# Optimization experiments

Measured on AMD Instinct MI355X. Metric: run time of the kernel, lower is better.

The kernel has to match this reference:

```python
import jax, jax.numpy as jnp
import numpy as np

B, C, N, T = 32, 32, 300, 64      # batch, residual/conv channels, nodes, seq_len
DIM, K, SKIP, GD = 40, 20, 64, 2  # node_dim, top-k (subgraph_size), skip_channels, gcn_depth
TANH_A, PROP_A = 3.0, 0.05
KSET = (2, 3, 6, 7)
TOUT = T - (KSET[-1] - 1)          # 58: time length after dilated inception (dilation=1)


def conv2d(x, w, b):
    y = jax.lax.conv_general_dilated(x, w, (1, 1), 'VALID', dimension_numbers=('NCHW', 'OIHW', 'NCHW'))
    return y + b[None, :, None, None]


def setup_inputs() -> dict:
    key = jax.random.key(0)
    ks = iter(jax.random.split(key, 48))
    def nrm(shape, s=1.0):
        return jax.random.normal(next(ks), shape, jnp.float32) * s
    inp = {
        'x': nrm((B, C, N, T)),
        'x_skip': nrm((B, SKIP, N, 1)),
        'idx': jnp.arange(N, dtype=jnp.int32),
        'emb1': nrm((N, DIM), 0.1), 'emb2': nrm((N, DIM), 0.1),
        'lin1_w': nrm((DIM, DIM), 0.15), 'lin1_b': jnp.zeros((DIM,), jnp.float32),
        'lin2_w': nrm((DIM, DIM), 0.15), 'lin2_b': jnp.zeros((DIM,), jnp.float32),
        'skip_w': nrm((SKIP, C, 1, TOUT), 0.05), 'skip_b': jnp.zeros((SKIP,), jnp.float32),
        'mp1_w': nrm((C, (GD + 1) * C, 1, 1), 0.1), 'mp1_b': jnp.zeros((C,), jnp.float32),
        'mp2_w': nrm((C, (GD + 1) * C, 1, 1), 0.1), 'mp2_b': jnp.zeros((C,), jnp.float32),
        'ln_w': jnp.ones((C, N, TOUT), jnp.float32), 'ln_b': jnp.zeros((C, N, TOUT), jnp.float32),
    }
    for k in KSET:
        inp[f'fw{k}'] = nrm((C // 4, C, 1, k), 0.1); inp[f'fb{k}'] = jnp.zeros((C // 4,), jnp.float32)
        inp[f'gw{k}'] = nrm((C // 4, C, 1, k), 0.1); inp[f'gb{k}'] = jnp.zeros((C // 4,), jnp.float32)
    return inp


def _forward(x, x_skip, idx, emb1, emb2, lin1_w, lin1_b, lin2_w, lin2_b,
             fws, gws, skip_w, skip_b, mp1_w, mp1_b, mp2_w, mp2_b, ln_w, ln_b):
    # --- GraphConstructor: learned sparse adjacency via tanh/relu/top-k/scatter ---
    n1 = jnp.tanh(TANH_A * (emb1[idx] @ lin1_w.T + lin1_b))
    n2 = jnp.tanh(TANH_A * (emb2[idx] @ lin2_w.T + lin2_b))
    a = n1 @ n2.T - n2 @ n1.T
    A = jax.nn.relu(jnp.tanh(TANH_A * a))
    _, cols = jax.lax.top_k(A, K)                               # [N, K] per-row top-k indices
    mask = jnp.zeros_like(A).at[jnp.arange(N)[:, None], cols].set(1.0)
    A = A * mask
    # --- DilatedInception filter/gate (Conv2d kernel (1,k), crop to shortest) ---
    Xf = jnp.tanh(jnp.concatenate([conv2d(x, w, b)[..., -TOUT:] for w, b in fws], axis=1))
    Xg = jax.nn.sigmoid(jnp.concatenate([conv2d(x, w, b)[..., -TOUT:] for w, b in gws], axis=1))
    X = Xf * Xg                                                 # dropout is identity (training=False)
    X_skip_out = conv2d(X, skip_w, skip_b) + x_skip             # [B, SKIP, N, 1]
    # --- MixProp graph diffusion over A and A^T ---
    def mixprop(Xin, Adj, w, b):
        Ah = Adj + jnp.eye(N, dtype=Adj.dtype)
        Ah = Ah / Ah.sum(1)[:, None]                            # row-normalize
        H, hops = Xin, [Xin]
        for _ in range(GD):
            H = PROP_A * Xin + (1.0 - PROP_A) * jnp.einsum('bcwt,vw->bcvt', H, Ah)
            hops.append(H)
        return conv2d(jnp.concatenate(hops, axis=1), w, b)      # 1x1 conv: (GD+1)*C -> C
    X = mixprop(X, A, mp1_w, mp1_b) + mixprop(X, A.T, mp2_w, mp2_b)
    X = X + x[..., -TOUT:]
    # --- LayerNorm over (C, N, TOUT) with node-indexed affine ---
    mu = X.mean(axis=(1, 2, 3), keepdims=True)
    var = ((X - mu) ** 2).mean(axis=(1, 2, 3), keepdims=True)
    Xn = (X - mu) * jax.lax.rsqrt(var + 1e-5)
    X = Xn * ln_w[:, idx, :][None] + ln_b[:, idx, :][None]
    return X, X_skip_out


def reference(x, x_skip, idx, emb1, emb2, lin1_w, lin1_b, lin2_w, lin2_b,
              fw2, fb2, fw3, fb3, fw6, fb6, fw7, fb7,
              gw2, gb2, gw3, gb3, gw6, gb6, gw7, gb7,
              skip_w, skip_b, mp1_w, mp1_b, mp2_w, mp2_b, ln_w, ln_b):
    fws = [(fw2, fb2), (fw3, fb3), (fw6, fb6), (fw7, fb7)]
    gws = [(gw2, gb2), (gw3, gb3), (gw6, gb6), (gw7, gb7)]
    return _forward(x, x_skip, idx, emb1, emb2, lin1_w, lin1_b, lin2_w, lin2_b,
                    fws, gws, skip_w, skip_b, mp1_w, mp1_b, mp2_w, mp2_b, ln_w, ln_b)
```

## Files before the change

kernel.cpp:

```cpp
#include <hip/hip_runtime.h>
#include <hip/hip_bf16.h>
#include <math.h>

typedef __hip_bfloat16 bf16;
typedef __attribute__((ext_vector_type(8))) short bf16x8;
typedef __attribute__((ext_vector_type(4))) float f32x4;

#define NB 32
#define NC 32
#define NNODE 300
#define NT 64
#define NDIM 40
#define KTOP 20
#define NSKIP 64
#define NTOUT 58
#define SLAB 17400
#define BSLAB 556800
#define XEL 17817600
#define PSLAB 2048
#define BPSLAB 614400
#define XPEL 19660800

__device__ __forceinline__ float b2f(bf16 v){ return __bfloat162float(v); }
__device__ __forceinline__ bf16 f2b(float v){ return __float2bfloat16(v); }
__device__ __forceinline__ float fsig(float x){ return 1.0f/(1.0f + __expf(-x)); }
__device__ __forceinline__ float ftanh(float x){ return 2.0f*fsig(2.0f*x) - 1.0f; }

__device__ __forceinline__ unsigned short bbits(float v){
  bf16 h = f2b(v); unsigned short s; __builtin_memcpy(&s, &h, 2); return s;
}

__device__ __forceinline__ uint4 pack8(const float f[8]){
  uint4 d;
  d.x = (unsigned)bbits(f[0]) | ((unsigned)bbits(f[1]) << 16);
  d.y = (unsigned)bbits(f[2]) | ((unsigned)bbits(f[3]) << 16);
  d.z = (unsigned)bbits(f[4]) | ((unsigned)bbits(f[5]) << 16);
  d.w = (unsigned)bbits(f[6]) | ((unsigned)bbits(f[7]) << 16);
  return d;
}

__device__ __forceinline__ void bv_swz(int bid, int& b, int& v){
  int xcd = bid & 7, i = bid >> 3;
  int nb = xcd*1200 + i;
  b = nb / NNODE; v = nb - b*NNODE;
}

__global__ void k_nodes(const float* __restrict__ emb1, const float* __restrict__ emb2,
                        const float* __restrict__ l1w, const float* __restrict__ l1b,
                        const float* __restrict__ l2w, const float* __restrict__ l2b,
                        const int* __restrict__ idxp,
                        float* __restrict__ n1, float* __restrict__ n2){
  int i = blockIdx.x; int d = threadIdx.x;
  if (d >= NDIM) return;
  int r = idxp[i];
  float a1 = l1b[d], a2 = l2b[d];
  for (int k=0;k<NDIM;++k){
    a1 = fmaf(emb1[r*NDIM+k], l1w[d*NDIM+k], a1);
    a2 = fmaf(emb2[r*NDIM+k], l2w[d*NDIM+k], a2);
  }
  n1[i*NDIM+d] = tanhf(3.0f*a1);
  n2[i*NDIM+d] = tanhf(3.0f*a2);
}

__global__ void __launch_bounds__(64) k_adjrow(const float* __restrict__ n1,
                                               const float* __restrict__ n2,
                                               float* __restrict__ Am){
  int i = blockIdx.x; int lane = threadIdx.x;
  __shared__ float rowo[NNODE];
  __shared__ float rowv[NNODE];
  __shared__ int   sel[NNODE];
  for (int j=lane;j<NNODE;j+=64){
    float a = 0.f;
    #pragma unroll
    for (int k=0;k<NDIM;++k){
      float a1 = n1[i*NDIM+k], a2 = n2[i*NDIM+k];
      a = fmaf(a1, n2[j*NDIM+k], a);
      a = fmaf(-a2, n1[j*NDIM+k], a);
    }
    float v = tanhf(3.0f*a);
    v = v > 0.f ? v : 0.f;
    rowo[j]=v; rowv[j]=v; sel[j]=0;
  }
  __syncthreads();
  for (int it=0; it<KTOP; ++it){
    float best = -1.f; int bi = 0x7fffffff;
    for (int j=lane;j<NNODE;j+=64){
      float v = rowv[j];
      if (v > best){ best=v; bi=j; }
    }
    #pragma unroll
    for (int off=32; off; off>>=1){
      float ov = __shfl_xor(best, off);
      int   oi = __shfl_xor(bi, off);
      if (ov > best || (ov == best && oi < bi)){ best=ov; bi=oi; }
    }
    if (lane==0){ sel[bi]=1; rowv[bi]=-2.f; }
    __syncthreads();
  }
  for (int j=lane;j<NNODE;j+=64)
    Am[i*NNODE+j] = sel[j] ? rowo[j] : 0.f;
}

__global__ void __launch_bounds__(64) k_norm(const float* __restrict__ Am, float* __restrict__ Ah){
  int r = blockIdx.x;
  int side = r >= 304; int v = side ? r - 304 : r;
  float* dst = Ah + (size_t)(side ? 304*304 : 0) + v*304;
  int lane = threadIdx.x;
  if (v >= NNODE){
    for (int w=lane; w<304; w+=64) dst[w] = 0.f;
    return;
  }
  float s = 0.f;
  for (int w=lane; w<NNODE; w+=64)
    s += side ? Am[w*NNODE + v] : Am[v*NNODE + w];
  #pragma unroll
  for (int off=32; off; off>>=1) s += __shfl_xor(s, off);
  float inv = 1.0f/(s + 1.0f);
  for (int w=lane; w<304; w+=64){
    float a = (w < NNODE) ? (side ? Am[w*NNODE + v] : Am[v*NNODE + w]) : 0.f;
    if (w == v) a += 1.0f;
    dst[w] = a*inv;
  }
}

__global__ void k_mpk(const float* __restrict__ Ah, bf16* __restrict__ Mpk){
  int id = blockIdx.x*blockDim.x + threadIdx.x;
  if (id >= 4*320*320) return;
  int pm = id / (320*320);
  int rem = id % (320*320);
  int v = rem / 320, w = rem % 320;
  int s = pm >> 1, m = pm & 1;
  float val = 0.f;
  if (v < 304 && w < 304){
    const float* A = Ah + (size_t)s*304*304;
    float a = A[v*304 + w];
    if (m == 0){
      val = 0.95f*a + (v==w ? 0.05f : 0.f);
    } else {
      float d = 0.f;
      for (int u=0; u<304; ++u) d = fmaf(A[v*304 + u], A[u*304 + w], d);
      val = 0.9025f*d + 0.0475f*a + (v==w ? 0.05f : 0.f);
    }
  }
  int vt16 = v >> 4, lv = v & 15, ks = w >> 5, g = (w >> 3) & 3, j = w & 7;
  int lane = g*16 + lv;
  Mpk[(((size_t)(pm*20 + vt16)*10 + ks)*64 + lane)*8 + j] = f2b(val);
}

__global__ void k_wpack2(const float* __restrict__ fw2,const float* __restrict__ fw3,
                         const float* __restrict__ fw6,const float* __restrict__ fw7,
                         const float* __restrict__ gw2,const float* __restrict__ gw3,
                         const float* __restrict__ gw6,const float* __restrict__ gw7,
                         const float* __restrict__ fb2,const float* __restrict__ fb3,
                         const float* __restrict__ fb6,const float* __restrict__ fb7,
                         const float* __restrict__ gb2,const float* __restrict__ gb3,
                         const float* __restrict__ gb6,const float* __restrict__ gb7,
                         bf16* __restrict__ wfA, float* __restrict__ biasPk){
  int T = blockIdx.x*blockDim.x + threadIdx.x;
  if (T < 14336){
    int j = T & 7;
    int q = T >> 3;
    int l = q & 63; q >>= 6;
    int ks = q % 7, mt = q / 7;
    int m = mt*16 + (l & 15);
    int k = ks*32 + (l >> 4)*8 + j;
    int c = m >> 1, path = m & 1;
    int cls = c >> 3, o = c & 7;
    int ic = k / 7, d = k - ic*7;
    int kk = (cls==0) ? 2 : (cls==1) ? 3 : (cls==2) ? 6 : 7;
    int tp = d - (7 - kk);
    float val = 0.f;
    if (tp >= 0){
      const float* w = (path==0)
        ? (cls==0?fw2:cls==1?fw3:cls==2?fw6:fw7)
        : (cls==0?gw2:cls==1?gw3:cls==2?gw6:gw7);
      val = w[(o*NC + ic)*kk + tp];
    }
    wfA[T] = f2b(val);
  } else if (T < 14336 + 32){
    int c = T - 14336;
    int cls = c >> 3, o = c & 7;
    const float* fb = cls==0?fb2:cls==1?fb3:cls==2?fb6:fb7;
    const float* gb = cls==0?gb2:cls==1?gb3:cls==2?gb6:gb7;
    biasPk[c*2]   = fb[o];
    biasPk[c*2+1] = gb[o];
  }
}

__global__ void k_wprepM(const float* __restrict__ m1w, const float* __restrict__ m2w,
                         const float* __restrict__ m1b, const float* __restrict__ m2b,
                         bf16* __restrict__ pkB0, bf16* __restrict__ pkB1,
                         float* __restrict__ biasSum){
  int id = blockIdx.x*blockDim.x + threadIdx.x;
  if (id < 3072){
    int j = id & 7, l = (id >> 3) & 63, q = id >> 9;
    int ks = q % 3, nt = q / 3;
    int k = (l >> 4)*8 + j;
    int c = nt*16 + (l & 15);
    float val;
    if      (ks == 0) val = m1w[c*96 + k] + m2w[c*96 + k];
    else if (ks == 1) val = m1w[c*96 + 32 + k];
    else              val = m1w[c*96 + 64 + k];
    pkB0[id] = f2b(val);
  } else if (id < 5120){
    int id2 = id - 3072;
    int j = id2 & 7, l = (id2 >> 3) & 63, q = id2 >> 9;
    int ks = q & 1, nt = q >> 1;
    int k = (l >> 4)*8 + j;
    int c = nt*16 + (l & 15);
    pkB1[id2] = f2b(ks==0 ? m2w[c*96 + 32 + k] : m2w[c*96 + 64 + k]);
  } else if (id < 5152){
    int c = id - 5120;
    biasSum[c] = m1b[c] + m2b[c];
  }
}

__global__ void k_wTb(const float* __restrict__ sw, bf16* __restrict__ wTb){
  int id = blockIdx.x*blockDim.x + threadIdx.x;
  if (id >= 131072) return;
  int j = id & 7, l = (id >> 3) & 63, q = id >> 9;
  int ks = q & 63, nt = q >> 6;
  int k = ks*32 + (l >> 4)*8 + j;
  int t = k >> 5, c = k & 31;
  int sc = nt*16 + (l & 15);
  float val = (t < NTOUT) ? sw[sc*1856 + c*NTOUT + t] : 0.f;
  wTb[id] = f2b(val);
}

__global__ void __launch_bounds__(256) k_incepM(const float* __restrict__ x,
    const bf16* __restrict__ wfA, const float* __restrict__ biasPk,
    bf16* __restrict__ Xp){
  __shared__ bf16 xsb[32*72];
  __shared__ uint4 xim2[28*64];
  int b, n; bv_swz(blockIdx.x, b, n);
  int bn = b*NNODE + n;
  int tid = threadIdx.x;
  {
    int c = tid >> 3, t0 = (tid & 7)*8;
    const float* src = x + ((size_t)(b*NC + c)*NNODE + n)*NT + t0;
    float4 v0 = *reinterpret_cast<const float4*>(src);
    float4 v1 = *reinterpret_cast<const float4*>(src + 4);
    float f[8] = {v0.x,v0.y,v0.z,v0.w,v1.x,v1.y,v1.z,v1.w};
    *reinterpret_cast<uint4*>(&xsb[c*72 + t0]) = pack8(f);
    if ((tid & 7) == 7)
      *reinterpret_cast<uint4*>(&xsb[c*72 + 64]) = make_uint4(0,0,0,0);
  }
  __syncthreads();
  #pragma unroll
  for (int i=0;i<7;++i){
    int pr = tid + i*256;
    int kb = pr >> 6, t = pr & 63;
    int k0 = kb*8;
    int ic = k0 / 7, d = k0 - ic*7;
    unsigned sh[8];
    #pragma unroll
    for (int j=0;j<8;++j){
      sh[j] = *reinterpret_cast<const unsigned short*>(&xsb[ic*72 + t + d]);
      ++d; if (d == 7){ d = 0; ++ic; }
    }
    xim2[kb*64 + t] = make_uint4(sh[0]|(sh[1]<<16), sh[2]|(sh[3]<<16),
                                 sh[4]|(sh[5]<<16), sh[6]|(sh[7]<<16));
  }
  __syncthreads();
  int lane = tid & 63;
  int mt = __builtin_amdgcn_readfirstlane(tid >> 6);
  bf16x8 wA[7];
  #pragma unroll
  for (int ks=0; ks<7; ++ks)
    wA[ks] = *reinterpret_cast<const bf16x8*>(wfA + (size_t)((mt*7 + ks)*64 + lane)*8);
  int g = lane >> 4;
  int c0 = mt*8 + 2*g;
  float4 bias2 = *reinterpret_cast<const float4*>(biasPk + c0*2);
  #pragma unroll
  for (int nt=0; nt<4; ++nt){
    int t = (lane & 15) + nt*16;
    f32x4 acc = {0.f, 0.f, 0.f, 0.f};
    #pragma unroll
    for (int ks=0; ks<7; ++ks){
      bf16x8 bfr = __builtin_bit_cast(bf16x8, xim2[(ks*4 + g)*64 + t]);
      acc = __builtin_amdgcn_mfma_f32_16x16x32_bf16(wA[ks], bfr, acc, 0, 0, 0);
    }
    bool act = t < NTOUT;
    float X0 = act ? (ftanh(acc[0] + bias2.x) * fsig(acc[1] + bias2.y)) : 0.f;
    float X1 = act ? (ftanh(acc[2] + bias2.z) * fsig(acc[3] + bias2.w)) : 0.f;
    unsigned pv = (unsigned)bbits(X0) | ((unsigned)bbits(X1) << 16);
    *reinterpret_cast<unsigned*>(Xp + (size_t)bn*PSLAB + t*32 + c0) = pv;
  }
}

__global__ void __launch_bounds__(256) k_xt(const bf16* __restrict__ Xp, bf16* __restrict__ XpT2){
  __shared__ unsigned short tile[64*66];
  int bid = blockIdx.x;
  int b = bid / 160, r = bid - b*160;
  int wt = r / 32, ctt2 = r - wt*32;
  int w0 = wt*64, ct0 = ctt2*64;
  int tid = threadIdx.x;
  #pragma unroll
  for (int p=0; p<2; ++p){
    int w_in = (tid >> 3) + p*32;
    int ct_in = (tid & 7)*8;
    int w = w0 + w_in;
    uint4 d = (w < NNODE)
      ? *reinterpret_cast<const uint4*>(Xp + (size_t)b*BPSLAB + (size_t)w*PSLAB + ct0 + ct_in)
      : make_uint4(0,0,0,0);
    unsigned short* t = tile + w_in*66 + ct_in;
    *reinterpret_cast<unsigned*>(t)     = d.x;
    *reinterpret_cast<unsigned*>(t + 2) = d.y;
    *reinterpret_cast<unsigned*>(t + 4) = d.z;
    *reinterpret_cast<unsigned*>(t + 6) = d.w;
  }
  __syncthreads();
  #pragma unroll
  for (int p=0; p<2; ++p){
    int ct_in = (tid >> 3) + p*32;
    int wq = tid & 7;
    unsigned short u[8];
    #pragma unroll
    for (int j=0;j<8;++j) u[j] = tile[(wq*8 + j)*66 + ct_in];
    uint4 d;
    d.x = (unsigned)u[0] | ((unsigned)u[1] << 16);
    d.y = (unsigned)u[2] | ((unsigned)u[3] << 16);
    d.z = (unsigned)u[4] | ((unsigned)u[5] << 16);
    d.w = (unsigned)u[6] | ((unsigned)u[7] << 16);
    int ct = ct0 + ct_in;
    int w = w0 + wq*8;
    int ks = w >> 5, w_in32 = w & 31;
    size_t addr = (((size_t)(b*16 + (ct >> 7))*10 + ks) << 12) + ((ct & 127) << 5) + w_in32;
    *reinterpret_cast<uint4*>(XpT2 + addr) = d;
  }
}

__global__ void __launch_bounds__(256) k_skipM(const bf16* __restrict__ Xp, const bf16* __restrict__ wTb,
      const float* __restrict__ skip_b, const float* __restrict__ x_skip, float* __restrict__ out){
  int bn0 = blockIdx.x * 16;
  int tid = threadIdx.x, lane = tid & 63;
  int nt = __builtin_amdgcn_readfirstlane(tid >> 6);
  int g = lane >> 4, col = lane & 15;
  const bf16* aptr = Xp + (size_t)(bn0 + col)*PSLAB + g*8;
  const bf16* bptr = wTb + ((size_t)nt*64*64 + lane)*8;
  f32x4 acc = {0.f, 0.f, 0.f, 0.f};
  #pragma unroll 4
  for (int ks=0; ks<64; ++ks){
    bf16x8 aF = *reinterpret_cast<const bf16x8*>(aptr + ks*32);
    bf16x8 bF = *reinterpret_cast<const bf16x8*>(bptr + (size_t)ks*512);
    acc = __builtin_amdgcn_mfma_f32_16x16x32_bf16(aF, bF, acc, 0, 0, 0);
  }
  int sc = nt*16 + col;
  float sb = skip_b[sc];
  #pragma unroll
  for (int r=0;r<4;++r){
    int bn = bn0 + g*4 + r;
    int b = bn / NNODE, n = bn - b*NNODE;
    size_t so = (size_t)b*NSKIP*NNODE + (size_t)sc*NNODE + n;
    out[(size_t)XEL + so] = acc[r] + sb + x_skip[so];
  }
}

__global__ void __launch_bounds__(256) k_hop(const bf16* __restrict__ XpT2,
    const bf16* __restrict__ Mpk, bf16* __restrict__ H1, bf16* __restrict__ H2, int pass){
  __shared__ unsigned short bst[128*72];
  __shared__ __align__(16) unsigned short outT[64*136];
  int bid = blockIdx.x;
  int xcd = bid & 7, i = bid >> 3;
  int nb = xcd*640 + i;
  int b = nb / 160; int r = nb - b*160;
  int m = r / 80; r -= m*80;
  int vt = r >> 4; int ctt = r & 15;
  int ct0 = ctt*128, v0 = vt*64;
  int tid = threadIdx.x, lane = tid & 63;
  int mt = __builtin_amdgcn_readfirstlane(tid >> 6);
  int g = lane >> 4, col = lane & 15;
  const bf16* mbase = Mpk + (((size_t)((pass*2 + m)*20 + vt*4 + mt)*10)*64 + lane)*8;
  bf16x8 aF[10];
  #pragma unroll
  for (int ks=0; ks<10; ++ks)
    aF[ks] = *reinterpret_cast<const bf16x8*>(mbase + (size_t)ks*512);
  const bf16* tb = XpT2 + (((size_t)(b*16 + ctt)*10) << 12);
  int s_ct = tid >> 2, s_w = (tid & 3)*8;
  f32x4 acc[8];
  #pragma unroll
  for (int nt=0; nt<8; ++nt) acc[nt] = (f32x4){0.f,0.f,0.f,0.f};
  for (int ks=0; ks<10; ++ks){
    __syncthreads();
    const bf16* src = tb + ((size_t)ks << 12);
    {
      uint4 d0 = *reinterpret_cast<const uint4*>(src + s_ct*32 + s_w);
      uint4 d1 = *reinterpret_cast<const uint4*>(src + (s_ct+64)*32 + s_w);
      *reinterpret_cast<uint4*>(bst + s_ct*72 + s_w)      = d0;
      *reinterpret_cast<uint4*>(bst + (s_ct+64)*72 + s_w) = d1;
    }
    __syncthreads();
    #pragma unroll
    for (int nt=0; nt<8; ++nt){
      bf16x8 bF = *reinterpret_cast<const bf16x8*>(bst + (nt*16 + col)*72 + g*8);
      acc[nt] = __builtin_amdgcn_mfma_f32_16x16x32_bf16(aF[ks], bF, acc[nt], 0, 0, 0);
    }
  }
  #pragma unroll
  for (int nt=0; nt<8; ++nt){
    #pragma unroll
    for (int r4=0; r4<4; ++r4)
      outT[(mt*16 + g*4 + r4)*136 + nt*16 + col] = bbits(acc[nt][r4]);
  }
  __syncthreads();
  bf16* Hout = (m == 0) ? H1 : H2;
  {
    int vl = tid >> 2, e = tid & 3;
    int v = v0 + vl;
    if (v < NNODE){
      bf16* dst = Hout + (size_t)b*BPSLAB + (size_t)v*PSLAB + ct0;
      #pragma unroll
      for (int h=0; h<4; ++h){
        int ctl = e*32 + h*8;
        uint4 d = *reinterpret_cast<const uint4*>(outT + vl*136 + ctl);
        *reinterpret_cast<uint4*>(dst + ctl) = d;
      }
    }
  }
}

__global__ void __launch_bounds__(256) k_fuse0(bf16* __restrict__ Xp,
    const bf16* __restrict__ H1, const bf16* __restrict__ H2,
    const bf16* __restrict__ pkB, const float* __restrict__ biasSum){
  int b, v; bv_swz(blockIdx.x, b, v);
  size_t vbase = (size_t)b*BPSLAB + (size_t)v*PSLAB;
  int tid = threadIdx.x, lane = tid & 63;
  int mt = __builtin_amdgcn_readfirstlane(tid >> 6);
  int g = lane >> 4, col = lane & 15;
  int tRow = mt*16 + col;
  bf16x8 aX = *reinterpret_cast<const bf16x8*>(Xp + vbase + tRow*32 + g*8);
  bf16x8 a1 = *reinterpret_cast<const bf16x8*>(H1 + vbase + tRow*32 + g*8);
  bf16x8 a2 = *reinterpret_cast<const bf16x8*>(H2 + vbase + tRow*32 + g*8);
  __syncthreads();
  int t0 = mt*16 + g*4;
  bf16* pp = Xp + vbase;
  #pragma unroll
  for (int nt=0; nt<2; ++nt){
    int c_out = nt*16 + col;
    float bv = biasSum[c_out];
    f32x4 acc = {bv, bv, bv, bv};
    bf16x8 w0 = *reinterpret_cast<const bf16x8*>(pkB + (size_t)((nt*3+0)*64 + lane)*8);
    bf16x8 w1 = *reinterpret_cast<const bf16x8*>(pkB + (size_t)((nt*3+1)*64 + lane)*8);
    bf16x8 w2 = *reinterpret_cast<const bf16x8*>(pkB + (size_t)((nt*3+2)*64 + lane)*8);
    acc = __builtin_amdgcn_mfma_f32_16x16x32_bf16(aX, w0, acc, 0, 0, 0);
    acc = __builtin_amdgcn_mfma_f32_16x16x32_bf16(a1, w1, acc, 0, 0, 0);
    acc = __builtin_amdgcn_mfma_f32_16x16x32_bf16(a2, w2, acc, 0, 0, 0);
    #pragma unroll
    for (int r=0;r<4;++r)
      pp[(t0 + r)*32 + c_out] = f2b(acc[r]);
  }
}

__global__ void __launch_bounds__(256) k_fuse1(const bf16* __restrict__ P,
    const bf16* __restrict__ H1, const bf16* __restrict__ H2,
    float* __restrict__ out, const float* __restrict__ x,
    const bf16* __restrict__ pkB, double* __restrict__ part2){
  __shared__ float redS[4], redS2[4];
  int b, v; bv_swz(blockIdx.x, b, v);
  size_t vbase = (size_t)b*BPSLAB + (size_t)v*PSLAB;
  int tid = threadIdx.x, lane = tid & 63;
  int mt = __builtin_amdgcn_readfirstlane(tid >> 6);
  int g = lane >> 4, col = lane & 15;
  int tRow = mt*16 + col;
  bf16x8 a1 = *reinterpret_cast<const bf16x8*>(H1 + vbase + tRow*32 + g*8);
  bf16x8 a2 = *reinterpret_cast<const bf16x8*>(H2 + vbase + tRow*32 + g*8);
  int t0 = mt*16 + g*4;
  const bf16* pp = P + vbase;
  float s = 0.f, s2 = 0.f;
  #pragma unroll
  for (int nt=0; nt<2; ++nt){
    int c_out = nt*16 + col;
    f32x4 acc = {0.f, 0.f, 0.f, 0.f};
    bf16x8 w0 = *reinterpret_cast<const bf16x8*>(pkB + (size_t)((nt*2+0)*64 + lane)*8);
    bf16x8 w1 = *reinterpret_cast<const bf16x8*>(pkB + (size_t)((nt*2+1)*64 + lane)*8);
    acc = __builtin_amdgcn_mfma_f32_16x16x32_bf16(a1, w0, acc, 0, 0, 0);
    acc = __builtin_amdgcn_mfma_f32_16x16x32_bf16(a2, w1, acc, 0, 0, 0);
    float* po = out + ((size_t)(b*NC + c_out)*NNODE + v)*NTOUT + t0;
    const float* rx = x + ((size_t)(b*NC + c_out)*NNODE + v)*NT + 6 + t0;
    if (t0 <= 54){
      float2 r0 = *reinterpret_cast<const float2*>(rx);
      float2 r1 = *reinterpret_cast<const float2*>(rx + 2);
      float f0 = b2f(pp[(t0+0)*32 + c_out]) + acc[0] + r0.x;
      float f1 = b2f(pp[(t0+1)*32 + c_out]) + acc[1] + r0.y;
      float f2v = b2f(pp[(t0+2)*32 + c_out]) + acc[2] + r1.x;
      float f3 = b2f(pp[(t0+3)*32 + c_out]) + acc[3] + r1.y;
      *reinterpret_cast<float2*>(po)     = make_float2(f0, f1);
      *reinterpret_cast<float2*>(po + 2) = make_float2(f2v, f3);
      s  += f0 + f1 + f2v + f3;
      s2 += f0*f0 + f1*f1 + f2v*f2v + f3*f3;
    } else if (t0 == 56){
      float2 r0 = *reinterpret_cast<const float2*>(rx);
      float f0 = b2f(pp[(t0+0)*32 + c_out]) + acc[0] + r0.x;
      float f1 = b2f(pp[(t0+1)*32 + c_out]) + acc[1] + r0.y;
      *reinterpret_cast<float2*>(po) = make_float2(f0, f1);
      s  += f0 + f1;
      s2 += f0*f0 + f1*f1;
    }
  }
  #pragma unroll
  for (int o=32; o; o>>=1){ s += __shfl_down(s, o); s2 += __shfl_down(s2, o); }
  if (lane == 0){ redS[mt] = s; redS2[mt] = s2; }
  __syncthreads();
  if (tid == 0){
    float as = redS[0]+redS[1]+redS[2]+redS[3];
    float as2 = redS2[0]+redS2[1]+redS2[2]+redS2[3];
    atomicAdd(&part2[b*2],   (double)as);
    atomicAdd(&part2[b*2+1], (double)as2);
  }
}

__global__ void k_lnfin(const double* __restrict__ part2, float* __restrict__ stats){
  int b = threadIdx.x; if (b >= 32) return;
  double s = part2[b*2], s2 = part2[b*2+1];
  double n = (double)BSLAB;
  double mean = s/n;
  double var = s2/n - mean*mean;
  stats[b*2]   = (float)mean;
  stats[b*2+1] = (float)(1.0/sqrt(var + 1e-5));
}

__global__ void __launch_bounds__(256) k_lnapply(float* __restrict__ out, const float* __restrict__ stats,
        const float* __restrict__ lnw, const float* __restrict__ lnb, const int* __restrict__ idxp){
  int o = blockIdx.x*256 + threadIdx.x;
  int t = o % NTOUT; int v = (o / NTOUT) % NNODE; int c = (o / SLAB) % NC; int b = o / BSLAB;
  float mean = stats[b*2], rstd = stats[b*2+1];
  int vn = idxp[v];
  float wv = lnw[((size_t)c*NNODE + vn)*NTOUT + t];
  float bv = lnb[((size_t)c*NNODE + vn)*NTOUT + t];
  float vx = out[o];
  out[o] = (vx - mean)*rstd*wv + bv;
}

extern "C" void kernel_launch(void* const* d_in, const int* in_sizes, int n_in,
                              void* d_out, int out_size, void* d_ws, size_t ws_size,
                              hipStream_t stream) {
  (void)in_sizes; (void)n_in; (void)out_size; (void)ws_size;
  const float* x     = (const float*)d_in[0];
  const float* xskip = (const float*)d_in[1];
  const int*   idxp  = (const int*)d_in[2];
  const float* emb1  = (const float*)d_in[3];
  const float* emb2  = (const float*)d_in[4];
  const float* l1w   = (const float*)d_in[5];
  const float* l1b   = (const float*)d_in[6];
  const float* l2w   = (const float*)d_in[7];
  const float* l2b   = (const float*)d_in[8];
  const float* skw   = (const float*)d_in[9];
  const float* skb   = (const float*)d_in[10];
  const float* m1w   = (const float*)d_in[11];
  const float* m1b   = (const float*)d_in[12];
  const float* m2w   = (const float*)d_in[13];
  const float* m2b   = (const float*)d_in[14];
  const float* lnw   = (const float*)d_in[15];
  const float* lnb   = (const float*)d_in[16];
  const float* fw2=(const float*)d_in[17]; const float* fb2=(const float*)d_in[18];
  const float* gw2=(const float*)d_in[19]; const float* gb2=(const float*)d_in[20];
  const float* fw3=(const float*)d_in[21]; const float* fb3=(const float*)d_in[22];
  const float* gw3=(const float*)d_in[23]; const float* gb3=(const float*)d_in[24];
  const float* fw6=(const float*)d_in[25]; const float* fb6=(const float*)d_in[26];
  const float* gw6=(const float*)d_in[27]; const float* gb6=(const float*)d_in[28];
  const float* fw7=(const float*)d_in[29]; const float* fb7=(const float*)d_in[30];
  const float* gw7=(const float*)d_in[31]; const float* gb7=(const float*)d_in[32];
  float* out = (float*)d_out;

  char* wsbase = (char*)d_ws;
  size_t cur = 0;
  auto alloc = [&](size_t bytes)->char*{
    char* p = wsbase + cur;
    cur = (cur + bytes + 255) & ~(size_t)255;
    return p;
  };
  bf16*  Xp   = (bf16*) alloc((size_t)XPEL*2);
  bf16*  H1   = (bf16*) alloc((size_t)XPEL*2);
  bf16*  H2   = (bf16*) alloc((size_t)XPEL*2);
  bf16*  XpT2 = (bf16*) alloc((size_t)NB*16*10*4096*2);
  float* n1   = (float*)alloc(12000*4);
  float* n2   = (float*)alloc(12000*4);
  float* Am   = (float*)alloc(90000*4);
  float* Ah   = (float*)alloc(2*304*304*4);
  bf16*  Mpk  = (bf16*) alloc((size_t)4*20*10*64*8*2);
  bf16*  wTb  = (bf16*) alloc(131072*2);
  bf16*  wfA  = (bf16*) alloc(14336*2);
  float* biasPk = (float*)alloc(64*4);
  bf16*  pkB0 = (bf16*) alloc(3072*2);
  bf16*  pkB1 = (bf16*) alloc(2048*2);
  float* biasSum = (float*)alloc(32*4);
  double* part2 = (double*)alloc(64*8);
  float* stats = (float*)alloc(64*4);

  hipMemsetAsync(part2, 0, 64*sizeof(double), stream);

  k_nodes <<<NNODE, 64, 0, stream>>>(emb1, emb2, l1w, l1b, l2w, l2b, idxp, n1, n2);
  k_adjrow<<<NNODE, 64, 0, stream>>>(n1, n2, Am);
  k_norm  <<<608, 64, 0, stream>>>(Am, Ah);
  k_mpk   <<<1600, 256, 0, stream>>>(Ah, Mpk);

  k_wpack2<<<57, 256, 0, stream>>>(fw2,fw3,fw6,fw7, gw2,gw3,gw6,gw7,
                                   fb2,fb3,fb6,fb7, gb2,gb3,gb6,gb7, wfA, biasPk);
  k_wprepM<<<21, 256, 0, stream>>>(m1w, m2w, m1b, m2b, pkB0, pkB1, biasSum);
  k_wTb   <<<512, 256, 0, stream>>>(skw, wTb);

  k_incepM<<<NB*NNODE, 256, 0, stream>>>(x, wfA, biasPk, Xp);

  k_xt<<<5120, 256, 0, stream>>>(Xp, XpT2);

  k_skipM<<<(NB*NNODE)/16, 256, 0, stream>>>(Xp, wTb, skb, xskip, out);

  k_hop  <<<5120, 256, 0, stream>>>(XpT2, Mpk, H1, H2, 0);
  k_fuse0<<<NB*NNODE, 256, 0, stream>>>(Xp, H1, H2, pkB0, biasSum);

  k_hop  <<<5120, 256, 0, stream>>>(XpT2, Mpk, H1, H2, 1);
  k_fuse1<<<NB*NNODE, 256, 0, stream>>>(Xp, H1, H2, out, x, pkB1, part2);

  k_lnfin<<<1, 32, 0, stream>>>(part2, stats);
  k_lnapply<<<XEL/256, 256, 0, stream>>>(out, stats, lnw, lnb, idxp);
}
```

Before: 443.8 us.

## Reorder inception GEMM K dimension to tap-major and drop im2col staging

The packed inception weights are reordered so the MFMA K index runs as (tap, channel) rather than channel*7+tap. The kernel can then read B fragments straight from a time-major, XOR-swizzled copy of the input in shared memory, with no im2col buffer. This removes one __syncthreads, the scalar 16-bit gather loop, and most of the LDS footprint. The cost is scattered 16-bit stores into shared memory when the swizzled input tile is built.

```diff
diff --git a/kernel.cpp b/kernel.cpp
--- a/kernel.cpp
+++ b/kernel.cpp
@@ -159,14 +159,13 @@
   int T = blockIdx.x*blockDim.x + threadIdx.x;
   if (T < 14336){
     int j = T & 7;
-    int q = T >> 3;
-    int l = q & 63; q >>= 6;
-    int ks = q % 7, mt = q / 7;
+    int l = (T >> 3) & 63;
+    int q = T >> 9;
+    int d = q % 7, mt = q / 7;
     int m = mt*16 + (l & 15);
-    int k = ks*32 + (l >> 4)*8 + j;
+    int ic = (l >> 4)*8 + j;
     int c = m >> 1, path = m & 1;
     int cls = c >> 3, o = c & 7;
-    int ic = k / 7, d = k - ic*7;
     int kk = (cls==0) ? 2 : (cls==1) ? 3 : (cls==2) ? 6 : 7;
     int tp = d - (7 - kk);
     float val = 0.f;
@@ -230,55 +229,47 @@
 __global__ void __launch_bounds__(256) k_incepM(const float* __restrict__ x,
     const bf16* __restrict__ wfA, const float* __restrict__ biasPk,
     bf16* __restrict__ Xp){
-  __shared__ bf16 xsb[32*72];
-  __shared__ uint4 xim2[28*64];
+  __shared__ unsigned short xcm[72*32];
   int b, n; bv_swz(blockIdx.x, b, n);
   int bn = b*NNODE + n;
   int tid = threadIdx.x;
   {
-    int c = tid >> 3, t0 = (tid & 7)*8;
+    int c = tid >> 3, tq = tid & 7, t0 = tq*8;
     const float* src = x + ((size_t)(b*NC + c)*NNODE + n)*NT + t0;
     float4 v0 = *reinterpret_cast<const float4*>(src);
     float4 v1 = *reinterpret_cast<const float4*>(src + 4);
     float f[8] = {v0.x,v0.y,v0.z,v0.w,v1.x,v1.y,v1.z,v1.w};
-    *reinterpret_cast<uint4*>(&xsb[c*72 + t0]) = pack8(f);
-    if ((tid & 7) == 7)
-      *reinterpret_cast<uint4*>(&xsb[c*72 + 64]) = make_uint4(0,0,0,0);
-  }
-  __syncthreads();
-  #pragma unroll
-  for (int i=0;i<7;++i){
-    int pr = tid + i*256;
-    int kb = pr >> 6, t = pr & 63;
-    int k0 = kb*8;
-    int ic = k0 / 7, d = k0 - ic*7;
-    unsigned sh[8];
-    #pragma unroll
-    for (int j=0;j<8;++j){
-      sh[j] = *reinterpret_cast<const unsigned short*>(&xsb[ic*72 + t + d]);
-      ++d; if (d == 7){ d = 0; ++ic; }
-    }
-    xim2[kb*64 + t] = make_uint4(sh[0]|(sh[1]<<16), sh[2]|(sh[3]<<16),
-                                 sh[4]|(sh[5]<<16), sh[6]|(sh[7]<<16));
+    int gl = c >> 3, cl = c & 7;
+    #pragma unroll
+    for (int i=0;i<8;++i){
+      int t = t0 + i;
+      int pg = gl ^ ((t >> 3) & 3);
+      xcm[t*32 + pg*8 + cl] = bbits(f[i]);
+    }
+    int zt = 64 + (tid >> 5), zic = tid & 31;
+    int zpg = (zic >> 3) ^ ((zt >> 3) & 3);
+    xcm[zt*32 + zpg*8 + (zic & 7)] = 0;
   }
   __syncthreads();
   int lane = tid & 63;
   int mt = __builtin_amdgcn_readfirstlane(tid >> 6);
   bf16x8 wA[7];
   #pragma unroll
-  for (int ks=0; ks<7; ++ks)
-    wA[ks] = *reinterpret_cast<const bf16x8*>(wfA + (size_t)((mt*7 + ks)*64 + lane)*8);
-  int g = lane >> 4;
+  for (int d=0; d<7; ++d)
+    wA[d] = *reinterpret_cast<const bf16x8*>(wfA + (size_t)((mt*7 + d)*64 + lane)*8);
+  int g = lane >> 4, col = lane & 15;
   int c0 = mt*8 + 2*g;
   float4 bias2 = *reinterpret_cast<const float4*>(biasPk + c0*2);
   #pragma unroll
   for (int nt=0; nt<4; ++nt){
-    int t = (lane & 15) + nt*16;
+    int t = col + nt*16;
     f32x4 acc = {0.f, 0.f, 0.f, 0.f};
     #pragma unroll
-    for (int ks=0; ks<7; ++ks){
-      bf16x8 bfr = __builtin_bit_cast(bf16x8, xim2[(ks*4 + g)*64 + t]);
-      acc = __builtin_amdgcn_mfma_f32_16x16x32_bf16(wA[ks], bfr, acc, 0, 0, 0);
+    for (int d=0; d<7; ++d){
+      int tr = t + d;
+      int pg = g ^ ((tr >> 3) & 3);
+      bf16x8 bfr = *reinterpret_cast<const bf16x8*>(&xcm[tr*32 + pg*8]);
+      acc = __builtin_amdgcn_mfma_f32_16x16x32_bf16(wA[d], bfr, acc, 0, 0, 0);
     }
     bool act = t < NTOUT;
     float X0 = act ? (ftanh(acc[0] + bias2.x) * fsig(acc[1] + bias2.y)) : 0.f;
```

Result: faster. 419.9 us (-5.4%).
